# Kernel tuning notes

Hardware: AMD Instinct MI355X
Metric: run time of the kernel (lower is better)

Reference implementation:

```python
import jax, jax.numpy as jnp
import numpy as np

D_IO = 512
D_MODEL = 1024
NUM_LAYERS = 3
SEQ = 2048
BATCH = 16


def _pos_encoding(seq_len, d_model, dtype):
    # matches torch PositionalEncoding buffer pe[:S] with shape [S, 1, d_model]
    position = jnp.arange(seq_len, dtype=jnp.float32)[:, None]
    div_term = jnp.exp(jnp.arange(0, d_model, 2, dtype=jnp.float32) * (-np.log(10000.0) / d_model))
    pe = jnp.zeros((seq_len, d_model), dtype=jnp.float32)
    pe = pe.at[:, 0::2].set(jnp.sin(position * div_term))
    pe = pe.at[:, 1::2].set(jnp.cos(position * div_term))
    return pe[:, None, :].astype(dtype)


def _kernel(x):
    return jax.nn.elu(x) + 1.0


def _lin_attn(x, Wq, Wk, Wv):
    # x: [S, B, d_model]; Wq/Wk: [d_key, d_model]; Wv: [d_model, d_model]
    Q = _kernel(x @ Wq.T)  # [S, B, d_key]
    K = _kernel(x @ Wk.T)  # [S, B, d_key]
    V = x @ Wv.T           # [S, B, d_model]
    d_key = Wq.shape[0]
    d_model = Wv.shape[0]
    B = x.shape[1]

    def step(carry, qkv):
        s, z = carry
        q, k, v = qkv  # [B,d_key], [B,d_key], [B,d_model]
        s = s + k.T @ v                 # [d_key, d_model] (note: sums over batch, as in source)
        z = z + k                       # [B, d_key]
        numer = q @ s                   # [B, d_model]
        denom = jnp.sum(q * z, axis=-1, keepdims=True)  # [B, 1]
        return (s, z), numer / denom

    init = (jnp.zeros((d_key, d_model), x.dtype), jnp.zeros((B, d_key), x.dtype))
    _, y = jax.lax.scan(step, init, (Q, K, V))
    return y  # [S, B, d_model]


def reference(x, in_W, in_b, Wq, Wk, Wv, h1_W, h1_b, h2_W, h2_b, out_W, out_b):
    h = jax.nn.relu(x @ in_W.T + in_b)
    h = h + _pos_encoding(x.shape[0], h.shape[-1], h.dtype)
    for l in range(Wq.shape[0]):  # fixed small num_layers
        x_t = _lin_attn(h, Wq[l], Wk[l], Wv[l]) + h
        x_t = jax.nn.relu(x_t @ h1_W[l].T + h1_b[l])
        x_t = x_t @ h2_W[l].T + h2_b[l]
        h = x_t + h
    return jax.nn.softmax(h @ out_W.T + out_b, axis=-1)


def setup_inputs() -> dict:
    key = jax.random.key(0)
    ks = jax.random.split(key, 12)
    s_io = 1.0 / np.sqrt(D_IO)
    s_m = 1.0 / np.sqrt(D_MODEL)
    L = NUM_LAYERS
    return {
        "x": jax.random.normal(ks[0], (SEQ, BATCH, D_IO), jnp.float32),
        "in_W": jax.random.normal(ks[1], (D_MODEL, D_IO), jnp.float32) * s_io,
        "in_b": jnp.zeros((D_MODEL,), jnp.float32),
        "Wq": jax.random.normal(ks[2], (L, D_MODEL, D_MODEL), jnp.float32) * s_m,
        "Wk": jax.random.normal(ks[3], (L, D_MODEL, D_MODEL), jnp.float32) * s_m,
        "Wv": jax.random.normal(ks[4], (L, D_MODEL, D_MODEL), jnp.float32) * s_m,
        "h1_W": jax.random.normal(ks[5], (L, D_MODEL, D_MODEL), jnp.float32) * s_m,
        "h1_b": jnp.zeros((L, D_MODEL), jnp.float32),
        "h2_W": jax.random.normal(ks[6], (L, D_MODEL, D_MODEL), jnp.float32) * s_m,
        "h2_b": jnp.zeros((L, D_MODEL), jnp.float32),
        "out_W": jax.random.normal(ks[7], (D_IO, D_MODEL), jnp.float32) * s_m,
        "out_b": jnp.zeros((D_IO,), jnp.float32),
    }
```

## Files before the change

### kernel.cpp

```cpp
#include <hip/hip_runtime.h>
#include <math.h>


#define SEQ    2048
#define NB     16
#define DIO    512
#define DM     1024
#define NLAYER 3
#define ROWS   (SEQ * NB)
#define LC     64
#define NCH    (SEQ / LC)
#define RC     (LC * NB)

typedef __attribute__((ext_vector_type(8))) short bf16x8;
typedef __attribute__((ext_vector_type(4))) float f32x4;

#if defined(__has_builtin)
#if __has_builtin(__builtin_amdgcn_global_load_lds)
#define HAS_GLL 1
#endif
#endif

__device__ __forceinline__ ushort f2bf(float f) {
    unsigned u = __float_as_uint(f);
    return (ushort)((u + 0x7fffu + ((u >> 16) & 1u)) >> 16);
}
__device__ __forceinline__ float bf2f(ushort h) {
    return __uint_as_float((unsigned)h << 16);
}
__device__ __forceinline__ void split2(float f, ushort& h, ushort& l) {
    h = f2bf(f);
    l = f2bf(f - bf2f(h));
}
__device__ __forceinline__ float rc1(ushort h, ushort l) {
    return bf2f(h) + bf2f(l);
}

template <int ACT, bool PE, bool CAUSAL, bool KLIM>
__global__ __launch_bounds__(256) void mgemm(
    const ushort* __restrict__ Ah, const ushort* __restrict__ Al,
    const ushort* __restrict__ Bh, const ushort* __restrict__ Bl,
    const float* __restrict__ bias,
    float* __restrict__ Cf, ushort* __restrict__ Ch, ushort* __restrict__ Cl,
    const float* __restrict__ Rf, int accf,
    int M, int N, int K, long sA, long sB, long sC)
{
    const int cz = blockIdx.z;
    Ah += (long)cz * sA; Al += (long)cz * sA;
    Bh += (long)cz * sB; Bl += (long)cz * sB;
    const long cbase = (long)cz * sC;

    const int nx = gridDim.x;
    const int lin = blockIdx.y * nx + blockIdx.x;
    const int chunkpx = (nx * gridDim.y) >> 3;
    const int nl = (lin & 7) * chunkpx + (lin >> 3);
    const int bm = nl / nx, bn = nl % nx;

    if (CAUSAL && bn > bm) return;

    const int tid = threadIdx.x;
    const int lane = tid & 63;
    const int wv = tid >> 6;
    const int wr = wv >> 1, wc = wv & 1;

    __shared__ ushort lds[4][4096];

    const ushort* gsrc = (wv == 0) ? Ah : (wv == 1) ? Al : (wv == 2) ? Bh : Bl;
    const long rowbase = (long)((wv < 2 ? bm : bn) * 128);

    const int kmax = KLIM ? (((bm + 1) * 128 < K) ? (bm + 1) * 128 : K) : K;

    const ushort* gp[8];
    {
        const int lr = lane >> 2, sst = lane & 3;
#pragma unroll
        for (int it = 0; it < 8; ++it) {
            int r = it * 16 + lr;
            int s = sst ^ ((r >> 1) & 3);
            gp[it] = gsrc + (rowbase + r) * (long)K + s * 8;
        }
    }

    f32x4 acc[4][4];
#pragma unroll
    for (int m = 0; m < 4; ++m)
#pragma unroll
        for (int n = 0; n < 4; ++n)
            acc[m][n] = (f32x4){0.f, 0.f, 0.f, 0.f};

    const int fr = lane & 15;
    const int sl = lane >> 4;

    for (int k0 = 0; k0 < kmax; k0 += 32) {
        __syncthreads();
#if HAS_GLL
#pragma unroll
        for (int it = 0; it < 8; ++it)
            __builtin_amdgcn_global_load_lds(
                (const __attribute__((address_space(1))) unsigned int*)(gp[it] + k0),
                (__attribute__((address_space(3))) unsigned int*)&lds[wv][it * 512],
                16, 0, 0);
#else
        uint4 tmp[8];
#pragma unroll
        for (int it = 0; it < 8; ++it) tmp[it] = *(const uint4*)(gp[it] + k0);
#pragma unroll
        for (int it = 0; it < 8; ++it)
            *(uint4*)&lds[wv][it * 512 + (lane << 3)] = tmp[it];
#endif
        __syncthreads();

        bf16x8 fah[4], fal[4], fbh[4], fbl[4];
#pragma unroll
        for (int m = 0; m < 4; ++m) {
            int row = wr * 64 + m * 16 + fr;
            int po = row * 32 + ((sl ^ ((row >> 1) & 3)) << 3);
            fah[m] = *(const bf16x8*)&lds[0][po];
            fal[m] = *(const bf16x8*)&lds[1][po];
        }
#pragma unroll
        for (int n = 0; n < 4; ++n) {
            int row = wc * 64 + n * 16 + fr;
            int po = row * 32 + ((sl ^ ((row >> 1) & 3)) << 3);
            fbh[n] = *(const bf16x8*)&lds[2][po];
            fbl[n] = *(const bf16x8*)&lds[3][po];
        }
#pragma unroll
        for (int m = 0; m < 4; ++m)
#pragma unroll
            for (int n = 0; n < 4; ++n) {
                acc[m][n] = __builtin_amdgcn_mfma_f32_16x16x32_bf16(fah[m], fbh[n], acc[m][n], 0, 0, 0);
                acc[m][n] = __builtin_amdgcn_mfma_f32_16x16x32_bf16(fah[m], fbl[n], acc[m][n], 0, 0, 0);
                acc[m][n] = __builtin_amdgcn_mfma_f32_16x16x32_bf16(fal[m], fbh[n], acc[m][n], 0, 0, 0);
            }
    }

    const long crow0 = (long)bm * 128 + wr * 64;
    const int ccol0 = bn * 128 + wc * 64;
#pragma unroll
    for (int m = 0; m < 4; ++m) {
#pragma unroll
        for (int q = 0; q < 4; ++q) {
            long row = crow0 + m * 16 + ((lane >> 4) << 2) + q;
            long rbase = cbase + row * (long)N;
#pragma unroll
            for (int n = 0; n < 4; ++n) {
                int col = ccol0 + n * 16 + (lane & 15);
                float v = acc[m][n][q];
                if (bias) v += bias[col];
                if (ACT == 1) v = fmaxf(v, 0.f);
                if (ACT == 2) v = (v > 0.f) ? v + 1.f : expf(v);
                if (PE) {
                    int t = (int)(row >> 4);
                    int ih = col >> 1;
                    float dv = expf((float)ih * (-9.210340371976184f / 512.0f));
                    float ang = (float)t * dv;
                    v += (col & 1) ? cosf(ang) : sinf(ang);
                }
                if (CAUSAL && ((col >> 4) > (int)(row >> 4))) v = 0.f;
                if (accf) v += Cf[rbase + col];
                if (Rf) v += Rf[rbase + col];
                if (Cf) Cf[rbase + col] = v;
                if (Ch) {
                    ushort hh, ll;
                    split2(v, hh, ll);
                    Ch[rbase + col] = hh;
                    Cl[rbase + col] = ll;
                }
            }
        }
    }
}

__global__ __launch_bounds__(256) void split_kernel(
    const float* __restrict__ s, ushort* __restrict__ h, ushort* __restrict__ l, long n)
{
    for (long i = ((long)blockIdx.x * 256 + threadIdx.x) * 4; i < n;
         i += (long)gridDim.x * 1024) {
        float4 v = *(const float4*)(s + i);
        ushort4 hh, ll;
        split2(v.x, hh.x, ll.x); split2(v.y, hh.y, ll.y);
        split2(v.z, hh.z, ll.z); split2(v.w, hh.w, ll.w);
        *(ushort4*)(h + i) = hh;
        *(ushort4*)(l + i) = ll;
    }
}

__global__ __launch_bounds__(256) void transpose_plane(
    const ushort* __restrict__ src, ushort* __restrict__ dst)
{
    long c = blockIdx.z;
    src += c * (long)RC * DM;
    dst += c * (long)DM * RC;
    int r0 = blockIdx.y * 32, c0 = blockIdx.x * 32;
    __shared__ ushort t[32][36];
    int tr = threadIdx.x >> 3, tc = (threadIdx.x & 7) * 4;
    ushort4 v = *(const ushort4*)(src + (long)(r0 + tr) * DM + c0 + tc);
    t[tr][tc] = v.x; t[tr][tc + 1] = v.y; t[tr][tc + 2] = v.z; t[tr][tc + 3] = v.w;
    __syncthreads();
    ushort4 o;
    o.x = t[tc + 0][tr]; o.y = t[tc + 1][tr]; o.z = t[tc + 2][tr]; o.w = t[tc + 3][tr];
    *(ushort4*)(dst + (long)(c0 + tr) * RC + r0 + tc) = o;
}

__global__ __launch_bounds__(256) void gprefix_split(
    const float* __restrict__ G, ushort* __restrict__ Gh, ushort* __restrict__ Gl)
{
    long e = ((long)blockIdx.x * 256 + threadIdx.x) * 4;
    float4 run = {0.f, 0.f, 0.f, 0.f};
    for (int c = 0; c < NCH; ++c) {
        long off = (long)c * DM * DM + e;
        float4 t = *(const float4*)(G + off);
        ushort4 hh, ll;
        split2(run.x, hh.x, ll.x); split2(run.y, hh.y, ll.y);
        split2(run.z, hh.z, ll.z); split2(run.w, hh.w, ll.w);
        *(ushort4*)(Gh + off) = hh;
        *(ushort4*)(Gl + off) = ll;
        run.x += t.x; run.y += t.y; run.z += t.z; run.w += t.w;
    }
}

__global__ __launch_bounds__(256) void zpart_kernel(
    const ushort* __restrict__ Kh, const ushort* __restrict__ Kl,
    float* __restrict__ Zp)
{
    int c = blockIdx.x, b = blockIdx.y;
    int d = threadIdx.x * 4;
    float4 acc = {0.f, 0.f, 0.f, 0.f};
    for (int t = 0; t < LC; ++t) {
        long row = (long)(c * LC + t) * NB + b;
        ushort4 h = *(const ushort4*)(Kh + row * DM + d);
        ushort4 l = *(const ushort4*)(Kl + row * DM + d);
        acc.x += rc1(h.x, l.x); acc.y += rc1(h.y, l.y);
        acc.z += rc1(h.z, l.z); acc.w += rc1(h.w, l.w);
    }
    *(float4*)(Zp + (long)(c * NB + b) * DM + d) = acc;
}

__global__ __launch_bounds__(256) void zprefix_kernel(float* __restrict__ Zp)
{
    int idx = blockIdx.x * 256 + threadIdx.x;
    int b = idx >> 8;
    int d = (idx & 255) * 4;
    float4 run = {0.f, 0.f, 0.f, 0.f};
    for (int c = 0; c < NCH; ++c) {
        float4* p = (float4*)(Zp + (long)(c * NB + b) * DM + d);
        float4 t = *p; *p = run;
        run.x += t.x; run.y += t.y; run.z += t.z; run.w += t.w;
    }
}

__global__ __launch_bounds__(256) void denom_kernel(
    const ushort* __restrict__ Qh, const ushort* __restrict__ Ql,
    const ushort* __restrict__ Kh, const ushort* __restrict__ Kl,
    const float* __restrict__ Zp, float* __restrict__ den)
{
    int wave = threadIdx.x >> 6, lane = threadIdx.x & 63;
    int cb = blockIdx.x * 4 + wave;
    int c = cb >> 4, b = cb & 15;
    float z[16];
    {
        const float* zp = Zp + (long)(c * NB + b) * DM + lane * 16;
#pragma unroll
        for (int i = 0; i < 16; ++i) z[i] = zp[i];
    }
    for (int t = 0; t < LC; ++t) {
        long ro = ((long)(c * LC + t) * NB + b) * DM + lane * 16;
        float p = 0.f;
#pragma unroll
        for (int g = 0; g < 4; ++g) {
            ushort4 kh = *(const ushort4*)(Kh + ro + g * 4);
            ushort4 kl = *(const ushort4*)(Kl + ro + g * 4);
            ushort4 qh = *(const ushort4*)(Qh + ro + g * 4);
            ushort4 ql = *(const ushort4*)(Ql + ro + g * 4);
            z[g * 4 + 0] += rc1(kh.x, kl.x);
            z[g * 4 + 1] += rc1(kh.y, kl.y);
            z[g * 4 + 2] += rc1(kh.z, kl.z);
            z[g * 4 + 3] += rc1(kh.w, kl.w);
            p += rc1(qh.x, ql.x) * z[g * 4 + 0] + rc1(qh.y, ql.y) * z[g * 4 + 1]
               + rc1(qh.z, ql.z) * z[g * 4 + 2] + rc1(qh.w, ql.w) * z[g * 4 + 3];
        }
#pragma unroll
        for (int off = 32; off > 0; off >>= 1) p += __shfl_down(p, off);
        if (lane == 0) den[(long)(c * LC + t) * NB + b] = p;
    }
}

__global__ __launch_bounds__(256) void attn_out_split(
    const float* __restrict__ numer, const float* __restrict__ h,
    const float* __restrict__ den, ushort* __restrict__ xh, ushort* __restrict__ xl)
{
    long e = ((long)blockIdx.x * 256 + threadIdx.x) * 4;
    int r = (int)(e >> 10);
    float d = den[r];
    float4 nv = *(const float4*)(numer + e);
    float4 hv = *(const float4*)(h + e);
    float v0 = nv.x / d + hv.x, v1 = nv.y / d + hv.y;
    float v2 = nv.z / d + hv.z, v3 = nv.w / d + hv.w;
    ushort4 hh, ll;
    split2(v0, hh.x, ll.x); split2(v1, hh.y, ll.y);
    split2(v2, hh.z, ll.z); split2(v3, hh.w, ll.w);
    *(ushort4*)(xh + e) = hh;
    *(ushort4*)(xl + e) = ll;
}

__global__ __launch_bounds__(256) void softmax_kernel(float* __restrict__ io)
{
    int wave = threadIdx.x >> 6, lane = threadIdx.x & 63;
    long row = (long)blockIdx.x * 4 + wave;
    float* p = io + row * DIO + lane * 8;
    float4 a = *(float4*)p, b = *(float4*)(p + 4);
    float m = fmaxf(fmaxf(fmaxf(a.x, a.y), fmaxf(a.z, a.w)),
                    fmaxf(fmaxf(b.x, b.y), fmaxf(b.z, b.w)));
#pragma unroll
    for (int off = 32; off > 0; off >>= 1) m = fmaxf(m, __shfl_xor(m, off));
    a.x = expf(a.x - m); a.y = expf(a.y - m); a.z = expf(a.z - m); a.w = expf(a.w - m);
    b.x = expf(b.x - m); b.y = expf(b.y - m); b.z = expf(b.z - m); b.w = expf(b.w - m);
    float s = a.x + a.y + a.z + a.w + b.x + b.y + b.z + b.w;
#pragma unroll
    for (int off = 32; off > 0; off >>= 1) s += __shfl_xor(s, off);
    float inv = 1.0f / s;
    a.x *= inv; a.y *= inv; a.z *= inv; a.w *= inv;
    b.x *= inv; b.y *= inv; b.z *= inv; b.w *= inv;
    *(float4*)p = a; *(float4*)(p + 4) = b;
}

#define F32BUF   134217728L
#define PLANE    67108864L
#define XPLANE   33554432L
#define WSMALL   1048576L
#define WBIG     6291456L
#define NEED     (2L*F32BUF + 16L*PLANE + 2L*XPLANE + 4L*WSMALL + 10L*WBIG + 131072L + 2097152L)

__device__ __attribute__((aligned(1024))) unsigned char g_ws[NEED];

extern "C" void kernel_launch(void* const* d_in, const int* in_sizes, int n_in,
                              void* d_out, int out_size, void* d_ws, size_t ws_size,
                              hipStream_t stream)
{
    const float* x    = (const float*)d_in[0];
    const float* in_W = (const float*)d_in[1];
    const float* in_b = (const float*)d_in[2];
    const float* Wq   = (const float*)d_in[3];
    const float* Wk   = (const float*)d_in[4];
    const float* Wv   = (const float*)d_in[5];
    const float* h1W  = (const float*)d_in[6];
    const float* h1b  = (const float*)d_in[7];
    const float* h2W  = (const float*)d_in[8];
    const float* h2b  = (const float*)d_in[9];
    const float* outW = (const float*)d_in[10];
    const float* outb = (const float*)d_in[11];
    float* out = (float*)d_out;

    unsigned char* base;
    if (ws_size >= (size_t)NEED) {
        base = (unsigned char*)d_ws;
    } else {
        static unsigned char* g_fb = nullptr;
        if (!g_fb) hipGetSymbolAddress((void**)&g_fb, HIP_SYMBOL(g_ws));
        base = g_fb;
    }

    unsigned char* p = base;
    float* hF  = (float*)p;  p += F32BUF;
    float* GtF = (float*)p;  p += F32BUF;
    ushort* hh  = (ushort*)p; p += PLANE;  ushort* hl  = (ushort*)p; p += PLANE;
    ushort* Qh  = (ushort*)p; p += PLANE;  ushort* Ql  = (ushort*)p; p += PLANE;
    ushort* Kh  = (ushort*)p; p += PLANE;  ushort* Kl  = (ushort*)p; p += PLANE;
    ushort* Vh  = (ushort*)p; p += PLANE;  ushort* Vl  = (ushort*)p; p += PLANE;
    ushort* Kth = (ushort*)p; p += PLANE;  ushort* Ktl = (ushort*)p; p += PLANE;
    ushort* Vth = (ushort*)p; p += PLANE;  ushort* Vtl = (ushort*)p; p += PLANE;
    ushort* Gth = (ushort*)p; p += PLANE;  ushort* Gtl = (ushort*)p; p += PLANE;
    ushort* Ph  = (ushort*)p; p += PLANE;  ushort* Pl  = (ushort*)p; p += PLANE;
    ushort* xh  = (ushort*)p; p += XPLANE; ushort* xl  = (ushort*)p; p += XPLANE;
    ushort* iWh = (ushort*)p; p += WSMALL; ushort* iWl = (ushort*)p; p += WSMALL;
    ushort* oWh = (ushort*)p; p += WSMALL; ushort* oWl = (ushort*)p; p += WSMALL;
    ushort* Wqh = (ushort*)p; p += WBIG;   ushort* Wql = (ushort*)p; p += WBIG;
    ushort* Wkh = (ushort*)p; p += WBIG;   ushort* Wkl = (ushort*)p; p += WBIG;
    ushort* Wvh = (ushort*)p; p += WBIG;   ushort* Wvl = (ushort*)p; p += WBIG;
    ushort* W1h = (ushort*)p; p += WBIG;   ushort* W1l = (ushort*)p; p += WBIG;
    ushort* W2h = (ushort*)p; p += WBIG;   ushort* W2l = (ushort*)p; p += WBIG;
    float* den = (float*)p;  p += 131072L;
    float* Zp  = (float*)p;  p += 2097152L;

    const long CS = (long)RC * DM;
    dim3 gFull(DM / 128, ROWS / 128);
    dim3 gChunk(DM / 128, RC / 128, NCH);
    dim3 gOut(DIO / 128, ROWS / 128);
    dim3 gTr(DM / 32, RC / 32, NCH);

    split_kernel<<<2048, 256, 0, stream>>>(x, xh, xl, (long)ROWS * DIO);
    split_kernel<<<2048, 256, 0, stream>>>(in_W, iWh, iWl, (long)DM * DIO);
    split_kernel<<<2048, 256, 0, stream>>>(outW, oWh, oWl, (long)DIO * DM);
    split_kernel<<<2048, 256, 0, stream>>>(Wq, Wqh, Wql, 3L * DM * DM);
    split_kernel<<<2048, 256, 0, stream>>>(Wk, Wkh, Wkl, 3L * DM * DM);
    split_kernel<<<2048, 256, 0, stream>>>(Wv, Wvh, Wvl, 3L * DM * DM);
    split_kernel<<<2048, 256, 0, stream>>>(h1W, W1h, W1l, 3L * DM * DM);
    split_kernel<<<2048, 256, 0, stream>>>(h2W, W2h, W2l, 3L * DM * DM);

    mgemm<1, true, false, false><<<gFull, 256, 0, stream>>>(
        xh, xl, iWh, iWl, in_b, hF, hh, hl, nullptr, 0,
        ROWS, DM, DIO, 0, 0, 0);

    for (int l = 0; l < NLAYER; ++l) {
        long wo = (long)l * DM * DM;

        mgemm<2, false, false, false><<<gFull, 256, 0, stream>>>(
            hh, hl, Wqh + wo, Wql + wo, nullptr, nullptr, Qh, Ql, nullptr, 0,
            ROWS, DM, DM, 0, 0, 0);
        mgemm<2, false, false, false><<<gFull, 256, 0, stream>>>(
            hh, hl, Wkh + wo, Wkl + wo, nullptr, nullptr, Kh, Kl, nullptr, 0,
            ROWS, DM, DM, 0, 0, 0);
        mgemm<0, false, false, false><<<gFull, 256, 0, stream>>>(
            hh, hl, Wvh + wo, Wvl + wo, nullptr, nullptr, Vh, Vl, nullptr, 0,
            ROWS, DM, DM, 0, 0, 0);

        transpose_plane<<<gTr, 256, 0, stream>>>(Kh, Kth);
        transpose_plane<<<gTr, 256, 0, stream>>>(Kl, Ktl);
        transpose_plane<<<gTr, 256, 0, stream>>>(Vh, Vth);
        transpose_plane<<<gTr, 256, 0, stream>>>(Vl, Vtl);

        mgemm<0, false, false, false><<<gChunk, 256, 0, stream>>>(
            Vth, Vtl, Kth, Ktl, nullptr, GtF, nullptr, nullptr, nullptr, 0,
            DM, DM, RC, CS, CS, CS);
        gprefix_split<<<1024, 256, 0, stream>>>(GtF, Gth, Gtl);

        mgemm<0, false, false, false><<<gChunk, 256, 0, stream>>>(
            Qh, Ql, Gth, Gtl, nullptr, GtF, nullptr, nullptr, nullptr, 0,
            RC, DM, DM, CS, CS, CS);
        mgemm<0, false, true, false><<<gChunk, 256, 0, stream>>>(
            Qh, Ql, Kh, Kl, nullptr, nullptr, Ph, Pl, nullptr, 0,
            RC, RC, DM, CS, CS, CS);
        mgemm<0, false, false, true><<<gChunk, 256, 0, stream>>>(
            Ph, Pl, Vth, Vtl, nullptr, GtF, nullptr, nullptr, nullptr, 1,
            RC, DM, RC, CS, CS, CS);

        zpart_kernel<<<dim3(NCH, NB), 256, 0, stream>>>(Kh, Kl, Zp);
        zprefix_kernel<<<NB, 256, 0, stream>>>(Zp);
        denom_kernel<<<128, 256, 0, stream>>>(Qh, Ql, Kh, Kl, Zp, den);

        attn_out_split<<<ROWS * (DM / 4) / 256, 256, 0, stream>>>(
            GtF, hF, den, Kth, Ktl);

        mgemm<1, false, false, false><<<gFull, 256, 0, stream>>>(
            Kth, Ktl, W1h + wo, W1l + wo, h1b + (long)l * DM,
            nullptr, Qh, Ql, nullptr, 0, ROWS, DM, DM, 0, 0, 0);
        mgemm<0, false, false, false><<<gFull, 256, 0, stream>>>(
            Qh, Ql, W2h + wo, W2l + wo, h2b + (long)l * DM,
            hF, hh, hl, hF, 0, ROWS, DM, DM, 0, 0, 0);
    }

    mgemm<0, false, false, false><<<gOut, 256, 0, stream>>>(
        hh, hl, oWh, oWl, outb, out, nullptr, nullptr, nullptr, 0,
        ROWS, DIO, DM, 0, 0, 0);
    softmax_kernel<<<ROWS / 4, 256, 0, stream>>>(out);
}
```

Measured before the change: 9.185 ms.

## Stage GEMM epilogue through LDS for coalesced stores; fuse attention output into PV GEMM

The GEMM epilogue now applies its elementwise ops in registers, then stages the bf16 hi/lo planes and the fp32 output through swizzled shared memory so each thread writes 16-byte vectors to global memory instead of scattered scalar stores. The PV GEMM gains an AOUT mode that adds the inter-chunk numerator, divides by the denominator, adds the residual and writes the split bf16 planes directly. This removes the separate attn_out_split pass and the fp32 numerator round trip. The denominator kernels are moved earlier so they run before the fused GEMM, and the epilogue now needs extra barriers and LDS traffic.

```diff
diff --git a/kernel.cpp b/kernel.cpp
--- a/kernel.cpp
+++ b/kernel.cpp
@@ -35,14 +35,20 @@
 __device__ __forceinline__ float rc1(ushort h, ushort l) {
     return bf2f(h) + bf2f(l);
 }
-
-template <int ACT, bool PE, bool CAUSAL, bool KLIM>
+__device__ __forceinline__ int sidx16(int r, int c) {
+    return r * 128 + ((((c >> 3) ^ (r & 15)) & 15) << 3) + (c & 7);
+}
+__device__ __forceinline__ int sidxf(int r, int c) {
+    return r * 128 + ((((c >> 2) ^ (r & 7)) & 31) << 2) + (c & 3);
+}
+
+template <int ACT, bool PE, bool CAUSAL, bool KLIM, bool AOUT>
 __global__ __launch_bounds__(256) void mgemm(
     const ushort* __restrict__ Ah, const ushort* __restrict__ Al,
     const ushort* __restrict__ Bh, const ushort* __restrict__ Bl,
     const float* __restrict__ bias,
     float* __restrict__ Cf, ushort* __restrict__ Ch, ushort* __restrict__ Cl,
-    const float* __restrict__ Rf, int accf,
+    const float* __restrict__ Rf, const float* __restrict__ den, int accf,
     int M, int N, int K, long sA, long sB, long sC)
 {
     const int cz = blockIdx.z;
@@ -63,7 +69,7 @@
     const int wv = tid >> 6;
     const int wr = wv >> 1, wc = wv & 1;
 
-    __shared__ ushort lds[4][4096];
+    __shared__ __align__(16) ushort lds[4][4096];
 
     const ushort* gsrc = (wv == 0) ? Ah : (wv == 1) ? Al : (wv == 2) ? Bh : Bl;
     const long rowbase = (long)((wv < 2 ? bm : bn) * 128);
@@ -135,38 +141,111 @@
             }
     }
 
-    const long crow0 = (long)bm * 128 + wr * 64;
-    const int ccol0 = bn * 128 + wc * 64;
+    const long growbase = (long)bm * 128;
+    const int gcolbase = bn * 128;
 #pragma unroll
     for (int m = 0; m < 4; ++m) {
 #pragma unroll
         for (int q = 0; q < 4; ++q) {
-            long row = crow0 + m * 16 + ((lane >> 4) << 2) + q;
-            long rbase = cbase + row * (long)N;
+            const int rl = wr * 64 + m * 16 + ((lane >> 4) << 2) + q;
+            const long grow = growbase + rl;
+            const long rbase = cbase + grow * (long)N;
 #pragma unroll
             for (int n = 0; n < 4; ++n) {
-                int col = ccol0 + n * 16 + (lane & 15);
+                const int cl = wc * 64 + n * 16 + (lane & 15);
+                const int col = gcolbase + cl;
                 float v = acc[m][n][q];
                 if (bias) v += bias[col];
                 if (ACT == 1) v = fmaxf(v, 0.f);
                 if (ACT == 2) v = (v > 0.f) ? v + 1.f : expf(v);
                 if (PE) {
-                    int t = (int)(row >> 4);
+                    int t = (int)(grow >> 4);
                     int ih = col >> 1;
                     float dv = expf((float)ih * (-9.210340371976184f / 512.0f));
                     float ang = (float)t * dv;
                     v += (col & 1) ? cosf(ang) : sinf(ang);
                 }
-                if (CAUSAL && ((col >> 4) > (int)(row >> 4))) v = 0.f;
-                if (accf) v += Cf[rbase + col];
-                if (Rf) v += Rf[rbase + col];
-                if (Cf) Cf[rbase + col] = v;
-                if (Ch) {
-                    ushort hh, ll;
-                    split2(v, hh, ll);
-                    Ch[rbase + col] = hh;
-                    Cl[rbase + col] = ll;
+                if (CAUSAL && ((col >> 4) > (int)(grow >> 4))) v = 0.f;
+                if (AOUT) {
+                    v = (v + Cf[rbase + col]) / den[(long)cz * RC + grow] + Rf[rbase + col];
+                } else {
+                    if (accf) v += Cf[rbase + col];
+                    if (Rf) v += Rf[rbase + col];
                 }
+                acc[m][n][q] = v;
+            }
+        }
+    }
+
+    ushort* LS = (ushort*)&lds[0][0];
+    if (Ch) {
+        __syncthreads();
+#pragma unroll
+        for (int m = 0; m < 4; ++m)
+#pragma unroll
+            for (int q = 0; q < 4; ++q) {
+                const int rl = wr * 64 + m * 16 + ((lane >> 4) << 2) + q;
+#pragma unroll
+                for (int n = 0; n < 4; ++n) {
+                    const int cl = wc * 64 + n * 16 + (lane & 15);
+                    LS[sidx16(rl, cl)] = f2bf(acc[m][n][q]);
+                }
+            }
+        __syncthreads();
+        {
+            const int r = tid >> 1, cb = (tid & 1) * 64;
+            long gof = cbase + (growbase + r) * (long)N + gcolbase + cb;
+#pragma unroll
+            for (int i = 0; i < 8; ++i)
+                *(uint4*)(Ch + gof + i * 8) = *(const uint4*)&LS[sidx16(r, cb + i * 8)];
+        }
+        __syncthreads();
+#pragma unroll
+        for (int m = 0; m < 4; ++m)
+#pragma unroll
+            for (int q = 0; q < 4; ++q) {
+                const int rl = wr * 64 + m * 16 + ((lane >> 4) << 2) + q;
+#pragma unroll
+                for (int n = 0; n < 4; ++n) {
+                    const int cl = wc * 64 + n * 16 + (lane & 15);
+                    float v = acc[m][n][q];
+                    ushort hh = f2bf(v);
+                    LS[sidx16(rl, cl)] = f2bf(v - bf2f(hh));
+                }
+            }
+        __syncthreads();
+        {
+            const int r = tid >> 1, cb = (tid & 1) * 64;
+            long gof = cbase + (growbase + r) * (long)N + gcolbase + cb;
+#pragma unroll
+            for (int i = 0; i < 8; ++i)
+                *(uint4*)(Cl + gof + i * 8) = *(const uint4*)&LS[sidx16(r, cb + i * 8)];
+        }
+    }
+    if (Cf && !AOUT) {
+        float* LF = (float*)&lds[0][0];
+        for (int half = 0; half < 2; ++half) {
+            __syncthreads();
+            if (wr == half) {
+#pragma unroll
+                for (int m = 0; m < 4; ++m)
+#pragma unroll
+                    for (int q = 0; q < 4; ++q) {
+                        const int rl = (wr * 64 + m * 16 + ((lane >> 4) << 2) + q) - half * 64;
+#pragma unroll
+                        for (int n = 0; n < 4; ++n) {
+                            const int cl = wc * 64 + n * 16 + (lane & 15);
+                            LF[sidxf(rl, cl)] = acc[m][n][q];
+                        }
+                    }
+            }
+            __syncthreads();
+            {
+                const int r = tid >> 2, cb = (tid & 3) * 32;
+                long gof = cbase + (growbase + half * 64 + r) * (long)N + gcolbase + cb;
+#pragma unroll
+                for (int i = 0; i < 8; ++i)
+                    *(float4*)(Cf + gof + i * 4) = *(const float4*)&LF[sidxf(r, cb + i * 4)];
             }
         }
     }
@@ -284,24 +363,6 @@
         for (int off = 32; off > 0; off >>= 1) p += __shfl_down(p, off);
         if (lane == 0) den[(long)(c * LC + t) * NB + b] = p;
     }
-}
-
-__global__ __launch_bounds__(256) void attn_out_split(
-    const float* __restrict__ numer, const float* __restrict__ h,
-    const float* __restrict__ den, ushort* __restrict__ xh, ushort* __restrict__ xl)
-{
-    long e = ((long)blockIdx.x * 256 + threadIdx.x) * 4;
-    int r = (int)(e >> 10);
-    float d = den[r];
-    float4 nv = *(const float4*)(numer + e);
-    float4 hv = *(const float4*)(h + e);
-    float v0 = nv.x / d + hv.x, v1 = nv.y / d + hv.y;
-    float v2 = nv.z / d + hv.z, v3 = nv.w / d + hv.w;
-    ushort4 hh, ll;
-    split2(v0, hh.x, ll.x); split2(v1, hh.y, ll.y);
-    split2(v2, hh.z, ll.z); split2(v3, hh.w, ll.w);
-    *(ushort4*)(xh + e) = hh;
-    *(ushort4*)(xl + e) = ll;
 }
 
 __global__ __launch_bounds__(256) void softmax_kernel(float* __restrict__ io)
@@ -398,21 +459,21 @@
     split_kernel<<<2048, 256, 0, stream>>>(h1W, W1h, W1l, 3L * DM * DM);
     split_kernel<<<2048, 256, 0, stream>>>(h2W, W2h, W2l, 3L * DM * DM);
 
-    mgemm<1, true, false, false><<<gFull, 256, 0, stream>>>(
-        xh, xl, iWh, iWl, in_b, hF, hh, hl, nullptr, 0,
+    mgemm<1, true, false, false, false><<<gFull, 256, 0, stream>>>(
+        xh, xl, iWh, iWl, in_b, hF, hh, hl, nullptr, nullptr, 0,
         ROWS, DM, DIO, 0, 0, 0);
 
     for (int l = 0; l < NLAYER; ++l) {
         long wo = (long)l * DM * DM;
 
-        mgemm<2, false, false, false><<<gFull, 256, 0, stream>>>(
-            hh, hl, Wqh + wo, Wql + wo, nullptr, nullptr, Qh, Ql, nullptr, 0,
+        mgemm<2, false, false, false, false><<<gFull, 256, 0, stream>>>(
+            hh, hl, Wqh + wo, Wql + wo, nullptr, nullptr, Qh, Ql, nullptr, nullptr, 0,
             ROWS, DM, DM, 0, 0, 0);
-        mgemm<2, false, false, false><<<gFull, 256, 0, stream>>>(
-            hh, hl, Wkh + wo, Wkl + wo, nullptr, nullptr, Kh, Kl, nullptr, 0,
+        mgemm<2, false, false, false, false><<<gFull, 256, 0, stream>>>(
+            hh, hl, Wkh + wo, Wkl + wo, nullptr, nullptr, Kh, Kl, nullptr, nullptr, 0,
             ROWS, DM, DM, 0, 0, 0);
-        mgemm<0, false, false, false><<<gFull, 256, 0, stream>>>(
-            hh, hl, Wvh + wo, Wvl + wo, nullptr, nullptr, Vh, Vl, nullptr, 0,
+        mgemm<0, false, false, false, false><<<gFull, 256, 0, stream>>>(
+            hh, hl, Wvh + wo, Wvl + wo, nullptr, nullptr, Vh, Vl, nullptr, nullptr, 0,
             ROWS, DM, DM, 0, 0, 0);
 
         transpose_plane<<<gTr, 256, 0, stream>>>(Kh, Kth);
@@ -420,38 +481,35 @@
         transpose_plane<<<gTr, 256, 0, stream>>>(Vh, Vth);
         transpose_plane<<<gTr, 256, 0, stream>>>(Vl, Vtl);
 
-        mgemm<0, false, false, false><<<gChunk, 256, 0, stream>>>(
-            Vth, Vtl, Kth, Ktl, nullptr, GtF, nullptr, nullptr, nullptr, 0,
-            DM, DM, RC, CS, CS, CS);
-        gprefix_split<<<1024, 256, 0, stream>>>(GtF, Gth, Gtl);
-
-        mgemm<0, false, false, false><<<gChunk, 256, 0, stream>>>(
-            Qh, Ql, Gth, Gtl, nullptr, GtF, nullptr, nullptr, nullptr, 0,
-            RC, DM, DM, CS, CS, CS);
-        mgemm<0, false, true, false><<<gChunk, 256, 0, stream>>>(
-            Qh, Ql, Kh, Kl, nullptr, nullptr, Ph, Pl, nullptr, 0,
-            RC, RC, DM, CS, CS, CS);
-        mgemm<0, false, false, true><<<gChunk, 256, 0, stream>>>(
-            Ph, Pl, Vth, Vtl, nullptr, GtF, nullptr, nullptr, nullptr, 1,
-            RC, DM, RC, CS, CS, CS);
-
         zpart_kernel<<<dim3(NCH, NB), 256, 0, stream>>>(Kh, Kl, Zp);
         zprefix_kernel<<<NB, 256, 0, stream>>>(Zp);
         denom_kernel<<<128, 256, 0, stream>>>(Qh, Ql, Kh, Kl, Zp, den);
 
-        attn_out_split<<<ROWS * (DM / 4) / 256, 256, 0, stream>>>(
-            GtF, hF, den, Kth, Ktl);
-
-        mgemm<1, false, false, false><<<gFull, 256, 0, stream>>>(
+        mgemm<0, false, false, false, false><<<gChunk, 256, 0, stream>>>(
+            Vth, Vtl, Kth, Ktl, nullptr, GtF, nullptr, nullptr, nullptr, nullptr, 0,
+            DM, DM, RC, CS, CS, CS);
+        gprefix_split<<<1024, 256, 0, stream>>>(GtF, Gth, Gtl);
+
+        mgemm<0, false, false, false, false><<<gChunk, 256, 0, stream>>>(
+            Qh, Ql, Gth, Gtl, nullptr, GtF, nullptr, nullptr, nullptr, nullptr, 0,
+            RC, DM, DM, CS, CS, CS);
+        mgemm<0, false, true, false, false><<<gChunk, 256, 0, stream>>>(
+            Qh, Ql, Kh, Kl, nullptr, nullptr, Ph, Pl, nullptr, nullptr, 0,
+            RC, RC, DM, CS, CS, CS);
+        mgemm<0, false, false, true, true><<<gChunk, 256, 0, stream>>>(
+            Ph, Pl, Vth, Vtl, nullptr, GtF, Kth, Ktl, hF, den, 0,
+            RC, DM, RC, CS, CS, CS);
+
+        mgemm<1, false, false, false, false><<<gFull, 256, 0, stream>>>(
             Kth, Ktl, W1h + wo, W1l + wo, h1b + (long)l * DM,
-            nullptr, Qh, Ql, nullptr, 0, ROWS, DM, DM, 0, 0, 0);
-        mgemm<0, false, false, false><<<gFull, 256, 0, stream>>>(
+            nullptr, Qh, Ql, nullptr, nullptr, 0, ROWS, DM, DM, 0, 0, 0);
+        mgemm<0, false, false, false, false><<<gFull, 256, 0, stream>>>(
             Qh, Ql, W2h + wo, W2l + wo, h2b + (long)l * DM,
-            hF, hh, hl, hF, 0, ROWS, DM, DM, 0, 0, 0);
-    }
-
-    mgemm<0, false, false, false><<<gOut, 256, 0, stream>>>(
-        hh, hl, oWh, oWl, outb, out, nullptr, nullptr, nullptr, 0,
+            hF, hh, hl, hF, nullptr, 0, ROWS, DM, DM, 0, 0, 0);
+    }
+
+    mgemm<0, false, false, false, false><<<gOut, 256, 0, stream>>>(
+        hh, hl, oWh, oWl, outb, out, nullptr, nullptr, nullptr, nullptr, 0,
         ROWS, DIO, DM, 0, 0, 0);
     softmax_kernel<<<ROWS / 4, 256, 0, stream>>>(out);
 }
```

Result: slower. 15.13 ms (+64.8%).

## Fuse attention output normalization into chunked GEMM epilogue and tune occupancy

Applied to the files above, without the earlier changes.

The elementwise attn_out_split kernel is removed. Its numer/den division, residual add and bf16 split now run in the epilogue of the final intra-chunk GEMM, with the denominator kernels moved earlier so den is ready. The GEMM also gets a min-blocks-per-CU launch bound and loads A fragments per m-iteration to reduce register pressure. This saves a full read/write pass over the activations per layer, at the risk of register spills from the tighter occupancy bound.

```diff
diff --git a/kernel.cpp b/kernel.cpp
--- a/kernel.cpp
+++ b/kernel.cpp
@@ -36,13 +36,13 @@
     return bf2f(h) + bf2f(l);
 }
 
-template <int ACT, bool PE, bool CAUSAL, bool KLIM>
-__global__ __launch_bounds__(256) void mgemm(
+template <int ACT, bool PE, bool CAUSAL, bool KLIM, bool AOUT>
+__global__ __launch_bounds__(256, 2) void mgemm(
     const ushort* __restrict__ Ah, const ushort* __restrict__ Al,
     const ushort* __restrict__ Bh, const ushort* __restrict__ Bl,
     const float* __restrict__ bias,
     float* __restrict__ Cf, ushort* __restrict__ Ch, ushort* __restrict__ Cl,
-    const float* __restrict__ Rf, int accf,
+    const float* __restrict__ Rf, const float* __restrict__ den, int accf,
     int M, int N, int K, long sA, long sB, long sC)
 {
     const int cz = blockIdx.z;
@@ -63,7 +63,7 @@
     const int wv = tid >> 6;
     const int wr = wv >> 1, wc = wv & 1;
 
-    __shared__ ushort lds[4][4096];
+    __shared__ __align__(16) ushort lds[4][4096];
 
     const ushort* gsrc = (wv == 0) ? Ah : (wv == 1) ? Al : (wv == 2) ? Bh : Bl;
     const long rowbase = (long)((wv < 2 ? bm : bn) * 128);
@@ -110,14 +110,7 @@
 #endif
         __syncthreads();
 
-        bf16x8 fah[4], fal[4], fbh[4], fbl[4];
-#pragma unroll
-        for (int m = 0; m < 4; ++m) {
-            int row = wr * 64 + m * 16 + fr;
-            int po = row * 32 + ((sl ^ ((row >> 1) & 3)) << 3);
-            fah[m] = *(const bf16x8*)&lds[0][po];
-            fal[m] = *(const bf16x8*)&lds[1][po];
-        }
+        bf16x8 fbh[4], fbl[4];
 #pragma unroll
         for (int n = 0; n < 4; ++n) {
             int row = wc * 64 + n * 16 + fr;
@@ -126,13 +119,18 @@
             fbl[n] = *(const bf16x8*)&lds[3][po];
         }
 #pragma unroll
-        for (int m = 0; m < 4; ++m)
+        for (int m = 0; m < 4; ++m) {
+            int row = wr * 64 + m * 16 + fr;
+            int po = row * 32 + ((sl ^ ((row >> 1) & 3)) << 3);
+            bf16x8 ah = *(const bf16x8*)&lds[0][po];
+            bf16x8 al = *(const bf16x8*)&lds[1][po];
 #pragma unroll
             for (int n = 0; n < 4; ++n) {
-                acc[m][n] = __builtin_amdgcn_mfma_f32_16x16x32_bf16(fah[m], fbh[n], acc[m][n], 0, 0, 0);
-                acc[m][n] = __builtin_amdgcn_mfma_f32_16x16x32_bf16(fah[m], fbl[n], acc[m][n], 0, 0, 0);
-                acc[m][n] = __builtin_amdgcn_mfma_f32_16x16x32_bf16(fal[m], fbh[n], acc[m][n], 0, 0, 0);
+                acc[m][n] = __builtin_amdgcn_mfma_f32_16x16x32_bf16(ah, fbh[n], acc[m][n], 0, 0, 0);
+                acc[m][n] = __builtin_amdgcn_mfma_f32_16x16x32_bf16(ah, fbl[n], acc[m][n], 0, 0, 0);
+                acc[m][n] = __builtin_amdgcn_mfma_f32_16x16x32_bf16(al, fbh[n], acc[m][n], 0, 0, 0);
             }
+        }
     }
 
     const long crow0 = (long)bm * 128 + wr * 64;
@@ -158,9 +156,13 @@
                     v += (col & 1) ? cosf(ang) : sinf(ang);
                 }
                 if (CAUSAL && ((col >> 4) > (int)(row >> 4))) v = 0.f;
-                if (accf) v += Cf[rbase + col];
-                if (Rf) v += Rf[rbase + col];
-                if (Cf) Cf[rbase + col] = v;
+                if (AOUT) {
+                    v = (v + Cf[rbase + col]) / den[(long)cz * RC + row] + Rf[rbase + col];
+                } else {
+                    if (accf) v += Cf[rbase + col];
+                    if (Rf) v += Rf[rbase + col];
+                }
+                if (Cf && !AOUT) Cf[rbase + col] = v;
                 if (Ch) {
                     ushort hh, ll;
                     split2(v, hh, ll);
@@ -284,24 +286,6 @@
         for (int off = 32; off > 0; off >>= 1) p += __shfl_down(p, off);
         if (lane == 0) den[(long)(c * LC + t) * NB + b] = p;
     }
-}
-
-__global__ __launch_bounds__(256) void attn_out_split(
-    const float* __restrict__ numer, const float* __restrict__ h,
-    const float* __restrict__ den, ushort* __restrict__ xh, ushort* __restrict__ xl)
-{
-    long e = ((long)blockIdx.x * 256 + threadIdx.x) * 4;
-    int r = (int)(e >> 10);
-    float d = den[r];
-    float4 nv = *(const float4*)(numer + e);
-    float4 hv = *(const float4*)(h + e);
-    float v0 = nv.x / d + hv.x, v1 = nv.y / d + hv.y;
-    float v2 = nv.z / d + hv.z, v3 = nv.w / d + hv.w;
-    ushort4 hh, ll;
-    split2(v0, hh.x, ll.x); split2(v1, hh.y, ll.y);
-    split2(v2, hh.z, ll.z); split2(v3, hh.w, ll.w);
-    *(ushort4*)(xh + e) = hh;
-    *(ushort4*)(xl + e) = ll;
 }
 
 __global__ __launch_bounds__(256) void softmax_kernel(float* __restrict__ io)
@@ -398,60 +382,57 @@
     split_kernel<<<2048, 256, 0, stream>>>(h1W, W1h, W1l, 3L * DM * DM);
     split_kernel<<<2048, 256, 0, stream>>>(h2W, W2h, W2l, 3L * DM * DM);
 
-    mgemm<1, true, false, false><<<gFull, 256, 0, stream>>>(
-        xh, xl, iWh, iWl, in_b, hF, hh, hl, nullptr, 0,
+    mgemm<1, true, false, false, false><<<gFull, 256, 0, stream>>>(
+        xh, xl, iWh, iWl, in_b, hF, hh, hl, nullptr, nullptr, 0,
         ROWS, DM, DIO, 0, 0, 0);
 
     for (int l = 0; l < NLAYER; ++l) {
         long wo = (long)l * DM * DM;
 
-        mgemm<2, false, false, false><<<gFull, 256, 0, stream>>>(
-            hh, hl, Wqh + wo, Wql + wo, nullptr, nullptr, Qh, Ql, nullptr, 0,
-            ROWS, DM, DM, 0, 0, 0);
-        mgemm<2, false, false, false><<<gFull, 256, 0, stream>>>(
-            hh, hl, Wkh + wo, Wkl + wo, nullptr, nullptr, Kh, Kl, nullptr, 0,
-            ROWS, DM, DM, 0, 0, 0);
-        mgemm<0, false, false, false><<<gFull, 256, 0, stream>>>(
-            hh, hl, Wvh + wo, Wvl + wo, nullptr, nullptr, Vh, Vl, nullptr, 0,
-            ROWS, DM, DM, 0, 0, 0);
+        mgemm<2, false, false, false, false><<<gFull, 256, 0, stream>>>(
+            hh, hl, Wqh + wo, Wql + wo, nullptr, nullptr, Qh, Ql,
+            nullptr, nullptr, 0, ROWS, DM, DM, 0, 0, 0);
+        mgemm<2, false, false, false, false><<<gFull, 256, 0, stream>>>(
+            hh, hl, Wkh + wo, Wkl + wo, nullptr, nullptr, Kh, Kl,
+            nullptr, nullptr, 0, ROWS, DM, DM, 0, 0, 0);
+        mgemm<0, false, false, false, false><<<gFull, 256, 0, stream>>>(
+            hh, hl, Wvh + wo, Wvl + wo, nullptr, nullptr, Vh, Vl,
+            nullptr, nullptr, 0, ROWS, DM, DM, 0, 0, 0);
 
         transpose_plane<<<gTr, 256, 0, stream>>>(Kh, Kth);
         transpose_plane<<<gTr, 256, 0, stream>>>(Kl, Ktl);
         transpose_plane<<<gTr, 256, 0, stream>>>(Vh, Vth);
         transpose_plane<<<gTr, 256, 0, stream>>>(Vl, Vtl);
 
-        mgemm<0, false, false, false><<<gChunk, 256, 0, stream>>>(
-            Vth, Vtl, Kth, Ktl, nullptr, GtF, nullptr, nullptr, nullptr, 0,
-            DM, DM, RC, CS, CS, CS);
-        gprefix_split<<<1024, 256, 0, stream>>>(GtF, Gth, Gtl);
-
-        mgemm<0, false, false, false><<<gChunk, 256, 0, stream>>>(
-            Qh, Ql, Gth, Gtl, nullptr, GtF, nullptr, nullptr, nullptr, 0,
-            RC, DM, DM, CS, CS, CS);
-        mgemm<0, false, true, false><<<gChunk, 256, 0, stream>>>(
-            Qh, Ql, Kh, Kl, nullptr, nullptr, Ph, Pl, nullptr, 0,
-            RC, RC, DM, CS, CS, CS);
-        mgemm<0, false, false, true><<<gChunk, 256, 0, stream>>>(
-            Ph, Pl, Vth, Vtl, nullptr, GtF, nullptr, nullptr, nullptr, 1,
-            RC, DM, RC, CS, CS, CS);
-
         zpart_kernel<<<dim3(NCH, NB), 256, 0, stream>>>(Kh, Kl, Zp);
         zprefix_kernel<<<NB, 256, 0, stream>>>(Zp);
         denom_kernel<<<128, 256, 0, stream>>>(Qh, Ql, Kh, Kl, Zp, den);
 
-        attn_out_split<<<ROWS * (DM / 4) / 256, 256, 0, stream>>>(
-            GtF, hF, den, Kth, Ktl);
-
-        mgemm<1, false, false, false><<<gFull, 256, 0, stream>>>(
+        mgemm<0, false, false, false, false><<<gChunk, 256, 0, stream>>>(
+            Vth, Vtl, Kth, Ktl, nullptr, GtF, nullptr, nullptr,
+            nullptr, nullptr, 0, DM, DM, RC, CS, CS, CS);
+        gprefix_split<<<1024, 256, 0, stream>>>(GtF, Gth, Gtl);
+
+        mgemm<0, false, false, false, false><<<gChunk, 256, 0, stream>>>(
+            Qh, Ql, Gth, Gtl, nullptr, GtF, nullptr, nullptr,
+            nullptr, nullptr, 0, RC, DM, DM, CS, CS, CS);
+        mgemm<0, false, true, false, false><<<gChunk, 256, 0, stream>>>(
+            Qh, Ql, Kh, Kl, nullptr, nullptr, Ph, Pl,
+            nullptr, nullptr, 0, RC, RC, DM, CS, CS, CS);
+        mgemm<0, false, false, true, true><<<gChunk, 256, 0, stream>>>(
+            Ph, Pl, Vth, Vtl, nullptr, GtF, Kth, Ktl,
+            hF, den, 0, RC, DM, RC, CS, CS, CS);
+
+        mgemm<1, false, false, false, false><<<gFull, 256, 0, stream>>>(
             Kth, Ktl, W1h + wo, W1l + wo, h1b + (long)l * DM,
-            nullptr, Qh, Ql, nullptr, 0, ROWS, DM, DM, 0, 0, 0);
-        mgemm<0, false, false, false><<<gFull, 256, 0, stream>>>(
+            nullptr, Qh, Ql, nullptr, nullptr, 0, ROWS, DM, DM, 0, 0, 0);
+        mgemm<0, false, false, false, false><<<gFull, 256, 0, stream>>>(
             Qh, Ql, W2h + wo, W2l + wo, h2b + (long)l * DM,
-            hF, hh, hl, hF, 0, ROWS, DM, DM, 0, 0, 0);
-    }
-
-    mgemm<0, false, false, false><<<gOut, 256, 0, stream>>>(
-        hh, hl, oWh, oWl, outb, out, nullptr, nullptr, nullptr, 0,
+            hF, hh, hl, hF, nullptr, 0, ROWS, DM, DM, 0, 0, 0);
+    }
+
+    mgemm<0, false, false, false, false><<<gOut, 256, 0, stream>>>(
+        hh, hl, oWh, oWl, outb, out, nullptr, nullptr, nullptr, nullptr, 0,
         ROWS, DIO, DM, 0, 0, 0);
     softmax_kernel<<<ROWS / 4, 256, 0, stream>>>(out);
 }
```

New measurement: 8.679 ms. 1.06x faster.
